# Kernel optimization log

Measured on AMD Instinct MI355X. Metric: run time of the kernel, lower is better.

The kernel has to match this reference:

```python
import jax, jax.numpy as jnp
import numpy as np

B, L, D, H = 2, 4096, 1024, 1  # head_dim == embed_dim in source, forcing H=1


def setup_inputs() -> dict:
    key = jax.random.key(0)
    k_x, kq, kk, kv, ko = jax.random.split(key, 5)
    s = 1.0 / np.sqrt(D)
    return {
        "x": jax.random.normal(k_x, (B, L, D), dtype=jnp.float32),
        "W_q": jax.random.normal(kq, (D, D), dtype=jnp.float32) * s,
        "W_k": jax.random.normal(kk, (D, D), dtype=jnp.float32) * s,
        "W_v": jax.random.normal(kv, (D, D), dtype=jnp.float32) * s,
        "W_o": jax.random.normal(ko, (D, D), dtype=jnp.float32) * s,
    }


def reference(x, W_q, W_k, W_v, W_o):
    # nn.Linear(y) = y @ W.T ; weights stored as (out, in)
    Hd = D  # head_dim = embed_dim (source quirk), so num_heads must be 1
    Q = jnp.einsum('bld,ed->ble', x, W_q).reshape(B, L, H, Hd).transpose(0, 2, 1, 3)
    K = jnp.einsum('bld,ed->ble', x, W_k).reshape(B, L, H, Hd).transpose(0, 2, 1, 3)
    V = jnp.einsum('bld,ed->ble', x, W_v).reshape(B, L, H, Hd).transpose(0, 2, 1, 3)
    scores = jnp.einsum('bhqd,bhkd->bhqk', Q, K) / jnp.sqrt(jnp.float32(Hd))
    attn = jax.nn.softmax(scores, axis=-1)
    out = jnp.einsum('bhqk,bhkd->bhqd', attn, V)  # (B,H,L,Hd)
    out = out.transpose(0, 2, 1, 3).reshape(B, L, D)
    return jnp.einsum('bld,ed->ble', out, W_o)
```

## Files before the change

### kernel.cpp

```cpp
#include <hip/hip_runtime.h>
#include <hip/hip_bf16.h>
#include <stdint.h>


typedef unsigned short u16;
typedef short short8 __attribute__((ext_vector_type(8)));
typedef float f32x4 __attribute__((ext_vector_type(4)));

__device__ __forceinline__ void async_ld16(void* lds, const void* g) {
  __builtin_amdgcn_global_load_lds(
      (const __attribute__((address_space(1))) unsigned int*)g,
      (__attribute__((address_space(3))) unsigned int*)lds,
      16, 0, 0);
}

__device__ __forceinline__ u16 f2bf(float f) {
  unsigned u = __float_as_uint(f);
  u += 0x7FFFu + ((u >> 16) & 1u);
  return (u16)(u >> 16);
}

__global__ __launch_bounds__(256)
void cast_f32_bf16(const float* __restrict__ in, u16* __restrict__ out, int n) {
  const int i = (blockIdx.x * 256 + threadIdx.x) * 8;
  if (i >= n) return;
  float4 a = ((const float4*)(in + i))[0];
  float4 b = ((const float4*)(in + i))[1];
  uint4 o;
  o.x = (unsigned)f2bf(a.x) | ((unsigned)f2bf(a.y) << 16);
  o.y = (unsigned)f2bf(a.z) | ((unsigned)f2bf(a.w) << 16);
  o.z = (unsigned)f2bf(b.x) | ((unsigned)f2bf(b.y) << 16);
  o.w = (unsigned)f2bf(b.z) | ((unsigned)f2bf(b.w) << 16);
  *(uint4*)(out + i) = o;
}

#define BM 128
#define BN 128
#define BK 32

template <int XSWZ>
__global__ __launch_bounds__(256)
void gemm_bt(const u16* __restrict__ A, const u16* __restrict__ Bt,
             void* __restrict__ Cv, int K, int lda, int ldb, int ldc,
             long long sAz, long long sBz, long long sCz,
             float scale, int store_f32) {
  __shared__ u16 As[2][BM * BK];
  __shared__ u16 Bs[2][BN * BK];

  int bx, by, bz;
  if constexpr (XSWZ) {
    const int gx = gridDim.x, gy = gridDim.y;
    const int nwg = gx * gy * gridDim.z;
    const int lin = (blockIdx.z * gy + blockIdx.y) * gx + blockIdx.x;
    const int chunk = nwg >> 3;
    const int swz = (lin & 7) * chunk + (lin >> 3);
    bx = swz % gx;
    const int t1 = swz / gx;
    by = t1 % gy;
    bz = t1 / gy;
  } else {
    bx = blockIdx.x; by = blockIdx.y; bz = blockIdx.z;
  }

  A  += (long long)bz * sAz;
  Bt += (long long)bz * sBz;

  const int tid  = threadIdx.x;
  const int wave = tid >> 6;
  const int lane = tid & 63;
  const int wm   = wave >> 1;
  const int wn   = wave & 1;
  const int r15  = lane & 15;
  const int q4   = lane >> 4;

  const int tileM = by * BM;
  const int tileN = bx * BN;

  const int srow = tid >> 2;
  const int scol = ((tid & 3) ^ (srow & 3)) * 8;

  const u16* Aptr = A + (long long)tileM * lda + scol;
  const u16* Bptr = Bt + (long long)tileN * ldb + scol;

  auto stage = [&](int kt) {
    const int k0 = kt * BK;
    u16* as = &As[kt & 1][tid * 8];
    u16* bs = &Bs[kt & 1][tid * 8];
    async_ld16(as,        Aptr + (long long)srow * lda + k0);
    async_ld16(as + 2048, Aptr + (long long)(srow + 64) * lda + k0);
    async_ld16(bs,        Bptr + (long long)srow * ldb + k0);
    async_ld16(bs + 2048, Bptr + (long long)(srow + 64) * ldb + k0);
  };

  f32x4 zero = {0.f, 0.f, 0.f, 0.f};
  f32x4 acc[4][4];
#pragma unroll
  for (int i = 0; i < 4; ++i)
#pragma unroll
    for (int j = 0; j < 4; ++j) acc[i][j] = zero;

  const int csw = ((q4 ^ (r15 & 3)) * 8);

  const int NT = K / BK;
  stage(0);
  if (NT > 1) stage(1);

  for (int kt = 0; kt < NT; ++kt) {
    if (kt + 1 < NT) asm volatile("s_waitcnt vmcnt(4)" ::: "memory");
    else             asm volatile("s_waitcnt vmcnt(0)" ::: "memory");
    __builtin_amdgcn_s_barrier();

    const u16* as = &As[kt & 1][0];
    const u16* bs = &Bs[kt & 1][0];

    short8 af[4], bf[4];
#pragma unroll
    for (int i = 0; i < 4; ++i)
      af[i] = *(const short8*)&as[(wm * 64 + i * 16 + r15) * BK + csw];
#pragma unroll
    for (int i = 0; i < 4; ++i)
      bf[i] = *(const short8*)&bs[(wn * 64 + i * 16 + r15) * BK + csw];

    __builtin_amdgcn_s_setprio(1);
#pragma unroll
    for (int i = 0; i < 4; ++i)
#pragma unroll
      for (int j = 0; j < 4; ++j)
        acc[i][j] = __builtin_amdgcn_mfma_f32_16x16x32_bf16(af[i], bf[j], acc[i][j], 0, 0, 0);
    __builtin_amdgcn_s_setprio(0);

    __builtin_amdgcn_s_barrier();
    if (kt + 2 < NT) stage(kt + 2);
  }

#pragma unroll
  for (int i = 0; i < 4; ++i) {
#pragma unroll
    for (int j = 0; j < 4; ++j) {
      const int col = tileN + wn * 64 + j * 16 + r15;
#pragma unroll
      for (int r = 0; r < 4; ++r) {
        const int row = tileM + wm * 64 + i * 16 + q4 * 4 + r;
        const long long idx = (long long)bz * sCz + (long long)row * ldc + col;
        const float val = acc[i][j][r] * scale;
        if (store_f32) ((float*)Cv)[idx] = val;
        else           ((u16*)Cv)[idx] = f2bf(val);
      }
    }
  }
}

__global__ __launch_bounds__(256)
void softmax_rows(u16* __restrict__ S) {
  const int tid = threadIdx.x;
  u16* rp = S + (long long)blockIdx.x * 4096;

  uint4 a = ((const uint4*)rp)[tid * 2];
  uint4 b = ((const uint4*)rp)[tid * 2 + 1];
  unsigned w[8] = {a.x, a.y, a.z, a.w, b.x, b.y, b.z, b.w};
  float v[16];
#pragma unroll
  for (int i = 0; i < 8; ++i) {
    v[2 * i]     = __uint_as_float(w[i] << 16);
    v[2 * i + 1] = __uint_as_float(w[i] & 0xFFFF0000u);
  }

  float m = v[0];
#pragma unroll
  for (int i = 1; i < 16; ++i) m = fmaxf(m, v[i]);
#pragma unroll
  for (int o = 32; o > 0; o >>= 1) m = fmaxf(m, __shfl_xor(m, o));
  __shared__ float redm[4];
  __shared__ float reds[4];
  const int wave = tid >> 6;
  if ((tid & 63) == 0) redm[wave] = m;
  __syncthreads();
  m = fmaxf(fmaxf(redm[0], redm[1]), fmaxf(redm[2], redm[3]));

  float s = 0.f;
#pragma unroll
  for (int i = 0; i < 16; ++i) {
    v[i] = __expf(v[i] - m);
    s += v[i];
  }
#pragma unroll
  for (int o = 32; o > 0; o >>= 1) s += __shfl_xor(s, o);
  if ((tid & 63) == 0) reds[wave] = s;
  __syncthreads();
  s = (reds[0] + reds[1]) + (reds[2] + reds[3]);
  const float inv = 1.0f / s;

#pragma unroll
  for (int i = 0; i < 8; ++i)
    w[i] = (unsigned)f2bf(v[2 * i] * inv) | ((unsigned)f2bf(v[2 * i + 1] * inv) << 16);
  uint4 oa = {w[0], w[1], w[2], w[3]};
  uint4 ob = {w[4], w[5], w[6], w[7]};
  ((uint4*)rp)[tid * 2] = oa;
  ((uint4*)rp)[tid * 2 + 1] = ob;
}

extern "C" void kernel_launch(void* const* d_in, const int* in_sizes, int n_in,
                              void* d_out, int out_size, void* d_ws, size_t ws_size,
                              hipStream_t stream) {
  const float* x  = (const float*)d_in[0];
  const float* Wq = (const float*)d_in[1];
  const float* Wk = (const float*)d_in[2];
  const float* Wv = (const float*)d_in[3];
  const float* Wo = (const float*)d_in[4];
  float* out = (float*)d_out;

  u16* xb  = (u16*)d_ws;
  u16* Wqb = xb  + 8388608;
  u16* Wkb = Wqb + 1048576;
  u16* Wvb = Wkb + 1048576;
  u16* Wob = Wvb + 1048576;
  u16* QKp = Wob + 1048576;
  u16* Vt  = QKp + 16777216;
  u16* S   = Vt  + 8388608;
  u16* O   = QKp;

  const dim3 blk(256);

  cast_f32_bf16<<<dim3(4096), blk, 0, stream>>>(x,  xb,  8388608);
  cast_f32_bf16<<<dim3(512),  blk, 0, stream>>>(Wq, Wqb, 1048576);
  cast_f32_bf16<<<dim3(512),  blk, 0, stream>>>(Wk, Wkb, 1048576);
  cast_f32_bf16<<<dim3(512),  blk, 0, stream>>>(Wv, Wvb, 1048576);
  cast_f32_bf16<<<dim3(512),  blk, 0, stream>>>(Wo, Wob, 1048576);

  gemm_bt<1><<<dim3(16, 64, 1), blk, 0, stream>>>(xb, Wqb, QKp,
                                                  1024, 1024, 1024, 2048,
                                                  0, 0, 0, 1.f, 0);
  gemm_bt<0><<<dim3(64, 8, 1), blk, 0, stream>>>(Wvb, xb, Vt,
                                                 1024, 1024, 1024, 8192,
                                                 0, 0, 0, 1.f, 0);
  gemm_bt<1><<<dim3(32, 32, 2), blk, 0, stream>>>(QKp, QKp + 1024, S,
                                                  1024, 2048, 2048, 4096,
                                                  8388608LL, 8388608LL, 16777216LL,
                                                  0.03125f, 0);
  softmax_rows<<<dim3(8192), blk, 0, stream>>>(S);
  gemm_bt<1><<<dim3(8, 32, 2), blk, 0, stream>>>(S, Vt, O,
                                                 4096, 4096, 8192, 1024,
                                                 16777216LL, 4096LL, 4194304LL,
                                                 1.f, 0);
  gemm_bt<1><<<dim3(8, 64, 1), blk, 0, stream>>>(O, Wob, out,
                                                 1024, 1024, 1024, 1024,
                                                 0, 0, 0, 1.f, 1);
}
```

Before: 398.7 us.

## Triple-buffer GEMM LDS pipeline and merge weight casts into one launch

The GEMM kernel moves from a double-buffered to a triple-buffered LDS ring and prefetches three K-tiles ahead, with vmcnt waits adjusted to match. The aim is to hide more global-load latency behind the MFMA work. The four separate weight-cast launches are folded into one kernel, removing three launch overheads. In exchange the GEMM uses more LDS (48KB per block), which could lower occupancy, and the modulo-3 buffer indexing adds a little per-iteration arithmetic.

```diff
diff --git a/kernel.cpp b/kernel.cpp
--- a/kernel.cpp
+++ b/kernel.cpp
@@ -34,6 +34,24 @@
   *(uint4*)(out + i) = o;
 }
 
+__global__ __launch_bounds__(256)
+void cast_w4_bf16(const float* __restrict__ w0, const float* __restrict__ w1,
+                  const float* __restrict__ w2, const float* __restrict__ w3,
+                  u16* __restrict__ out) {
+  const int idx = (blockIdx.x * 256 + threadIdx.x) * 8;
+  const int which = idx >> 20;
+  const int off = idx & 1048575;
+  const float* src = which == 0 ? w0 : which == 1 ? w1 : which == 2 ? w2 : w3;
+  float4 a = ((const float4*)(src + off))[0];
+  float4 b = ((const float4*)(src + off))[1];
+  uint4 o;
+  o.x = (unsigned)f2bf(a.x) | ((unsigned)f2bf(a.y) << 16);
+  o.y = (unsigned)f2bf(a.z) | ((unsigned)f2bf(a.w) << 16);
+  o.z = (unsigned)f2bf(b.x) | ((unsigned)f2bf(b.y) << 16);
+  o.w = (unsigned)f2bf(b.z) | ((unsigned)f2bf(b.w) << 16);
+  *(uint4*)(out + idx) = o;
+}
+
 #define BM 128
 #define BN 128
 #define BK 32
@@ -44,8 +62,8 @@
              void* __restrict__ Cv, int K, int lda, int ldb, int ldc,
              long long sAz, long long sBz, long long sCz,
              float scale, int store_f32) {
-  __shared__ u16 As[2][BM * BK];
-  __shared__ u16 Bs[2][BN * BK];
+  __shared__ u16 As[3][BM * BK];
+  __shared__ u16 Bs[3][BN * BK];
 
   int bx, by, bz;
   if constexpr (XSWZ) {
@@ -83,9 +101,10 @@
   const u16* Bptr = Bt + (long long)tileN * ldb + scol;
 
   auto stage = [&](int kt) {
+    const int b = kt % 3;
     const int k0 = kt * BK;
-    u16* as = &As[kt & 1][tid * 8];
-    u16* bs = &Bs[kt & 1][tid * 8];
+    u16* as = &As[b][tid * 8];
+    u16* bs = &Bs[b][tid * 8];
     async_ld16(as,        Aptr + (long long)srow * lda + k0);
     async_ld16(as + 2048, Aptr + (long long)(srow + 64) * lda + k0);
     async_ld16(bs,        Bptr + (long long)srow * ldb + k0);
@@ -104,14 +123,18 @@
   const int NT = K / BK;
   stage(0);
   if (NT > 1) stage(1);
+  if (NT > 2) stage(2);
 
   for (int kt = 0; kt < NT; ++kt) {
-    if (kt + 1 < NT) asm volatile("s_waitcnt vmcnt(4)" ::: "memory");
-    else             asm volatile("s_waitcnt vmcnt(0)" ::: "memory");
+    const int rem = NT - 1 - kt;
+    if (rem >= 2)      asm volatile("s_waitcnt vmcnt(8)" ::: "memory");
+    else if (rem == 1) asm volatile("s_waitcnt vmcnt(4)" ::: "memory");
+    else               asm volatile("s_waitcnt vmcnt(0)" ::: "memory");
     __builtin_amdgcn_s_barrier();
 
-    const u16* as = &As[kt & 1][0];
-    const u16* bs = &Bs[kt & 1][0];
+    const int b = kt % 3;
+    const u16* as = &As[b][0];
+    const u16* bs = &Bs[b][0];
 
     short8 af[4], bf[4];
 #pragma unroll
@@ -130,7 +153,7 @@
     __builtin_amdgcn_s_setprio(0);
 
     __builtin_amdgcn_s_barrier();
-    if (kt + 2 < NT) stage(kt + 2);
+    if (kt + 3 < NT) stage(kt + 3);
   }
 
 #pragma unroll
@@ -221,11 +244,8 @@
 
   const dim3 blk(256);
 
-  cast_f32_bf16<<<dim3(4096), blk, 0, stream>>>(x,  xb,  8388608);
-  cast_f32_bf16<<<dim3(512),  blk, 0, stream>>>(Wq, Wqb, 1048576);
-  cast_f32_bf16<<<dim3(512),  blk, 0, stream>>>(Wk, Wkb, 1048576);
-  cast_f32_bf16<<<dim3(512),  blk, 0, stream>>>(Wv, Wvb, 1048576);
-  cast_f32_bf16<<<dim3(512),  blk, 0, stream>>>(Wo, Wob, 1048576);
+  cast_f32_bf16<<<dim3(4096), blk, 0, stream>>>(x, xb, 8388608);
+  cast_w4_bf16<<<dim3(2048), blk, 0, stream>>>(Wq, Wk, Wv, Wo, Wqb);
 
   gemm_bt<1><<<dim3(16, 64, 1), blk, 0, stream>>>(xb, Wqb, QKp,
                                                   1024, 1024, 1024, 2048,
```

Result: no change. 396.9 us (-0.5%).
